# Kernel optimization log

Measured on AMD Instinct MI355X. Metric: run time of the kernel, lower is better.

## Reference

```python
import jax, jax.numpy as jnp
import numpy as np
from jax import lax


def setup_inputs() -> dict:
    key = jax.random.key(0)
    k1, k2 = jax.random.split(key)
    N, dim, m = 8192, 1024, 1024
    x = jax.random.normal(k1, (N, dim), dtype=jnp.float32)
    vectors = jax.random.normal(k2, (m, dim), dtype=jnp.float32) * 0.01
    bias = jnp.zeros((dim,), dtype=jnp.float32)
    return {"x": x, "vectors": vectors, "bias": bias}


def reference(x, vectors, bias):
    # Normalize each reflection vector to unit length: [m, d]
    v_normed = vectors / jnp.linalg.norm(vectors, axis=1, keepdims=True)

    def step(out, v):
        # out: [N, d], v: [d]
        proj = out @ v                       # [N]
        out = out - 2.0 * proj[:, None] * v  # rank-1 Householder update
        return out, None

    out, _ = lax.scan(step, x, v_normed)
    return out + bias
```

## Files before the change

kernel.cpp:

```cpp
#include <hip/hip_runtime.h>
#include <hip/hip_bf16.h>

typedef __attribute__((ext_vector_type(8))) short short8;
typedef __attribute__((ext_vector_type(4))) short s16x4;
typedef __attribute__((ext_vector_type(4))) float f32x4;

static __device__ inline short f2bf(float f) {
    unsigned u = __float_as_uint(f);
    unsigned r = (u + 0x7fffu + ((u >> 16) & 1u)) >> 16;
    return (short)r;
}
static __device__ inline float bf2f(short h) {
    return __uint_as_float(((unsigned)(unsigned short)h) << 16);
}

static __device__ inline int swz32(int row, int slot) {
    return row * 32 + ((slot ^ ((row >> 1) & 3)) << 3);
}
static __device__ inline int swz64(int row, int slot) {
    return row * 64 + ((slot ^ (row & 7)) << 3);
}

__global__ __launch_bounds__(256) void k_normalize(const float* __restrict__ vec,
                                                   float* __restrict__ V, int dim) {
    int row = blockIdx.x;
    const float4* src = (const float4*)(vec + (size_t)row * dim);
    float4* dst = (float4*)(V + (size_t)row * dim);
    int nv4 = dim >> 2;
    float ss = 0.f;
    for (int i = threadIdx.x; i < nv4; i += blockDim.x) {
        float4 v = src[i];
        ss += v.x * v.x + v.y * v.y + v.z * v.z + v.w * v.w;
    }
    for (int off = 32; off; off >>= 1) ss += __shfl_down(ss, off, 64);
    __shared__ float ws_[4];
    int lane = threadIdx.x & 63, w = threadIdx.x >> 6;
    if (lane == 0) ws_[w] = ss;
    __syncthreads();
    float inv = 1.0f / sqrtf(ws_[0] + ws_[1] + ws_[2] + ws_[3]);
    for (int i = threadIdx.x; i < nv4; i += blockDim.x) {
        float4 v = src[i];
        v.x *= inv; v.y *= inv; v.z *= inv; v.w *= inv;
        dst[i] = v;
    }
}

__global__ __launch_bounds__(256) void k_split(const float* __restrict__ X,
                                               short* __restrict__ Xh,
                                               short* __restrict__ Xl, int n4) {
    for (int i = blockIdx.x * blockDim.x + threadIdx.x; i < n4; i += gridDim.x * blockDim.x) {
        float4 v = ((const float4*)X)[i];
        float f[4] = {v.x, v.y, v.z, v.w};
        s16x4 h, l;
#pragma unroll
        for (int q = 0; q < 4; ++q) {
            h[q] = f2bf(f[q]);
            l[q] = f2bf(f[q] - bf2f(h[q]));
        }
        *(s16x4*)&Xh[(size_t)i * 4] = h;
        *(s16x4*)&Xl[(size_t)i * 4] = l;
    }
}

__global__ __launch_bounds__(256) void k_cast(const float* __restrict__ X,
                                              short* __restrict__ Xh, int n4) {
    for (int i = blockIdx.x * blockDim.x + threadIdx.x; i < n4; i += gridDim.x * blockDim.x) {
        float4 v = ((const float4*)X)[i];
        float f[4] = {v.x, v.y, v.z, v.w};
        s16x4 h;
#pragma unroll
        for (int q = 0; q < 4; ++q) h[q] = f2bf(f[q]);
        *(s16x4*)&Xh[(size_t)i * 4] = h;
    }
}

__global__ __launch_bounds__(256) void k_tsplit(const float* __restrict__ X,
                                                short* __restrict__ Xth,
                                                short* __restrict__ Xtl, int R, int C) {
    __shared__ float tile[32][33];
    int c0 = blockIdx.x * 32, r0 = blockIdx.y * 32;
    int t = threadIdx.x;
    int r = t >> 3, c4 = (t & 7) * 4;
    float4 v = *(const float4*)&X[(size_t)(r0 + r) * C + c0 + c4];
    tile[r][c4 + 0] = v.x; tile[r][c4 + 1] = v.y;
    tile[r][c4 + 2] = v.z; tile[r][c4 + 3] = v.w;
    __syncthreads();
    int rr = t >> 3, cc4 = (t & 7) * 4;
    s16x4 h, l;
#pragma unroll
    for (int q = 0; q < 4; ++q) {
        float f = tile[cc4 + q][rr];
        h[q] = f2bf(f);
        l[q] = f2bf(f - bf2f(h[q]));
    }
    *(s16x4*)&Xth[(size_t)(c0 + rr) * R + r0 + cc4] = h;
    *(s16x4*)&Xtl[(size_t)(c0 + rr) * R + r0 + cc4] = l;
}

template<int MODE, int TRI>
__global__ __launch_bounds__(256) void k_nt64(
    const short* __restrict__ Ah, const short* __restrict__ Al,
    const short* __restrict__ Bh, const short* __restrict__ Bl,
    float* __restrict__ Cf, short* __restrict__ Ch, short* __restrict__ Cl,
    int K, int lda, int ldb, int ldc) {
    __shared__ short As[2][64 * 32];
    __shared__ short Bs[2][64 * 32];
    int i0 = blockIdx.y * 64, j0 = blockIdx.x * 64;
    if (TRI == 2 && j0 < i0) return;
    int KE = (TRI == 1) ? (j0 + 64) : K;
    int t = threadIdx.x, lane = t & 63, wave = t >> 6;
    int wr = wave >> 1, wc = wave & 1;
    int srow = t >> 2, slot = t & 3;
    int sofs = swz32(srow, slot);
    int gofs = slot * 8;
    f32x4 acc[2][2] = {};
    for (int k0 = 0; k0 < KE; k0 += 32) {
        __syncthreads();
        *(short8*)&As[0][sofs] = *(const short8*)&Ah[(size_t)(i0 + srow) * lda + k0 + gofs];
        *(short8*)&As[1][sofs] = *(const short8*)&Al[(size_t)(i0 + srow) * lda + k0 + gofs];
        *(short8*)&Bs[0][sofs] = *(const short8*)&Bh[(size_t)(j0 + srow) * ldb + k0 + gofs];
        *(short8*)&Bs[1][sofs] = *(const short8*)&Bl[(size_t)(j0 + srow) * ldb + k0 + gofs];
        __syncthreads();
        int g = lane >> 4;
        short8 ah[2], al2[2], bh[2], bl2[2];
#pragma unroll
        for (int i = 0; i < 2; ++i) {
            int ro = swz32(wr * 32 + i * 16 + (lane & 15), g);
            ah[i] = *(const short8*)&As[0][ro];
            al2[i] = *(const short8*)&As[1][ro];
        }
#pragma unroll
        for (int j = 0; j < 2; ++j) {
            int ro = swz32(wc * 32 + j * 16 + (lane & 15), g);
            bh[j] = *(const short8*)&Bs[0][ro];
            bl2[j] = *(const short8*)&Bs[1][ro];
        }
#pragma unroll
        for (int i = 0; i < 2; ++i)
#pragma unroll
            for (int j = 0; j < 2; ++j) {
                acc[i][j] = __builtin_amdgcn_mfma_f32_16x16x32_bf16(ah[i], bh[j], acc[i][j], 0, 0, 0);
                acc[i][j] = __builtin_amdgcn_mfma_f32_16x16x32_bf16(ah[i], bl2[j], acc[i][j], 0, 0, 0);
                acc[i][j] = __builtin_amdgcn_mfma_f32_16x16x32_bf16(al2[i], bh[j], acc[i][j], 0, 0, 0);
            }
    }
#pragma unroll
    for (int i = 0; i < 2; ++i)
#pragma unroll
        for (int j = 0; j < 2; ++j) {
            int row0 = i0 + wr * 32 + i * 16 + ((lane >> 4) << 2);
            int col = j0 + wc * 32 + j * 16 + (lane & 15);
#pragma unroll
            for (int r = 0; r < 4; ++r) {
                float v = acc[i][j][r];
                size_t idx = (size_t)(row0 + r) * ldc + col;
                if (MODE == 2) {
                    Ch[idx] = f2bf((((row0 + r) == col) ? 1.f : 0.f) - v);
                } else {
                    short h = f2bf(v);
                    short l = f2bf(v - bf2f(h));
                    Ch[idx] = h;
                    Cl[idx] = l;
                    if (MODE == 3) Cf[idx] = v;
                }
            }
        }
}

__global__ __launch_bounds__(256) void k_baseinv2(const float* __restrict__ G,
                                                  short* __restrict__ Th, short* __restrict__ Tl,
                                                  short* __restrict__ Tth, short* __restrict__ Ttl,
                                                  int m) {
    __shared__ float Rs[64 * 64];
    int d = blockIdx.x >> 4, g = blockIdx.x & 15;
    int b0 = d * 64;
    int t = threadIdx.x, lane = t & 63, wave = t >> 6;
    {
        int r = t >> 2, c00 = (t & 3) * 16;
#pragma unroll
        for (int q = 0; q < 4; ++q)
            *(float4*)&Rs[r * 64 + c00 + q * 4] =
                *(const float4*)&G[(size_t)(b0 + r) * m + b0 + c00 + q * 4];
    }
    __syncthreads();
    int c = g * 4 + wave;
    float x = 0.f;
    for (int r = c; r >= 0; --r) {
        float prod = Rs[r * 64 + lane] * x;
        float s = prod;
#pragma unroll
        for (int off = 32; off; off >>= 1) s += __shfl_xor(s, off, 64);
        if (lane == r) x = ((r == c) ? 2.f : 0.f) - 2.f * s;
    }
    short h = f2bf(x);
    short l = f2bf(x - bf2f(h));
    Th[(size_t)(b0 + lane) * m + b0 + c] = h;
    Tl[(size_t)(b0 + lane) * m + b0 + c] = l;
    Tth[(size_t)(b0 + c) * m + b0 + lane] = h;
    Ttl[(size_t)(b0 + c) * m + b0 + lane] = l;
}

template<int PHASE>
__global__ __launch_bounds__(256) void k_trimm(
    const short* __restrict__ Ah, const short* __restrict__ Al,
    const short* __restrict__ Bh, const short* __restrict__ Bl,
    short* __restrict__ C1h, short* __restrict__ C1l,
    short* __restrict__ C2h, short* __restrict__ C2l,
    int m, int s) {
    __shared__ short As[2][64 * 32];
    __shared__ short Bs[2][64 * 32];
    int p = blockIdx.z;
    int a0 = 2 * p * s, c0 = a0 + s;
    int r0 = blockIdx.y * 64, ct = blockIdx.x * 64;
    int KS = (PHASE == 1) ? 0 : r0;
    int KE = (PHASE == 1) ? (ct + 64) : s;
    size_t tbase = (size_t)p * s * s;
    int t = threadIdx.x, lane = t & 63, wave = t >> 6;
    int wr = wave >> 1, wc = wave & 1;
    int srow = t >> 2, slot = t & 3;
    int sofs = swz32(srow, slot);
    int gofs = slot * 8;
    f32x4 acc[2][2] = {};
    for (int k0 = KS; k0 < KE; k0 += 32) {
        __syncthreads();
        if (PHASE == 1) {
            *(short8*)&As[0][sofs] = *(const short8*)&Ah[(size_t)(a0 + r0 + srow) * m + c0 + k0 + gofs];
            *(short8*)&As[1][sofs] = *(const short8*)&Al[(size_t)(a0 + r0 + srow) * m + c0 + k0 + gofs];
            *(short8*)&Bs[0][sofs] = *(const short8*)&Bh[(size_t)(c0 + ct + srow) * m + c0 + k0 + gofs];
            *(short8*)&Bs[1][sofs] = *(const short8*)&Bl[(size_t)(c0 + ct + srow) * m + c0 + k0 + gofs];
        } else {
            *(short8*)&As[0][sofs] = *(const short8*)&Ah[(size_t)(a0 + r0 + srow) * m + a0 + k0 + gofs];
            *(short8*)&As[1][sofs] = *(const short8*)&Al[(size_t)(a0 + r0 + srow) * m + a0 + k0 + gofs];
            *(short8*)&Bs[0][sofs] = *(const short8*)&Bh[tbase + (size_t)(ct + srow) * s + k0 + gofs];
            *(short8*)&Bs[1][sofs] = *(const short8*)&Bl[tbase + (size_t)(ct + srow) * s + k0 + gofs];
        }
        __syncthreads();
        int g = lane >> 4;
        short8 ah[2], al2[2], bh[2], bl2[2];
#pragma unroll
        for (int i = 0; i < 2; ++i) {
            int ro = swz32(wr * 32 + i * 16 + (lane & 15), g);
            ah[i] = *(const short8*)&As[0][ro];
            al2[i] = *(const short8*)&As[1][ro];
        }
#pragma unroll
        for (int j = 0; j < 2; ++j) {
            int ro = swz32(wc * 32 + j * 16 + (lane & 15), g);
            bh[j] = *(const short8*)&Bs[0][ro];
            bl2[j] = *(const short8*)&Bs[1][ro];
        }
#pragma unroll
        for (int i = 0; i < 2; ++i)
#pragma unroll
            for (int j = 0; j < 2; ++j) {
                acc[i][j] = __builtin_amdgcn_mfma_f32_16x16x32_bf16(ah[i], bh[j], acc[i][j], 0, 0, 0);
                acc[i][j] = __builtin_amdgcn_mfma_f32_16x16x32_bf16(ah[i], bl2[j], acc[i][j], 0, 0, 0);
                acc[i][j] = __builtin_amdgcn_mfma_f32_16x16x32_bf16(al2[i], bh[j], acc[i][j], 0, 0, 0);
            }
    }
#pragma unroll
    for (int i = 0; i < 2; ++i)
#pragma unroll
        for (int j = 0; j < 2; ++j) {
            int row0 = r0 + wr * 32 + i * 16 + ((lane >> 4) << 2);
            int col = ct + wc * 32 + j * 16 + (lane & 15);
#pragma unroll
            for (int r = 0; r < 4; ++r) {
                if (PHASE == 1) {
                    float v = acc[i][j][r];
                    short h = f2bf(v);
                    short l = f2bf(v - bf2f(h));
                    size_t idx = tbase + (size_t)col * s + row0 + r;
                    C1h[idx] = h;
                    C1l[idx] = l;
                } else {
                    float v = -acc[i][j][r];
                    short h = f2bf(v);
                    short l = f2bf(v - bf2f(h));
                    int R = a0 + row0 + r, Cc = c0 + col;
                    C1h[(size_t)R * m + Cc] = h;
                    C1l[(size_t)R * m + Cc] = l;
                    C2h[(size_t)Cc * m + R] = h;
                    C2l[(size_t)Cc * m + R] = l;
                }
            }
        }
}

__global__ __launch_bounds__(256) void k_apply3(const short* __restrict__ xh,
                                                const short* __restrict__ Qt,
                                                const float* __restrict__ bias,
                                                float* __restrict__ out, int dim) {
    __shared__ short As[128 * 64];
    __shared__ short Bs[128 * 64];
    int m0 = blockIdx.y * 128, n0 = blockIdx.x * 128;
    int t = threadIdx.x, lane = t & 63, wave = t >> 6;
    int wr = wave >> 1, wc = wave & 1;
    int sr = lane >> 3;
    int sslot = (lane & 7) ^ (sr & 7);
    f32x4 acc[4][4] = {};
    for (int k0 = 0; k0 < dim; k0 += 64) {
        __syncthreads();
#pragma unroll
        for (int q = 0; q < 4; ++q) {
            int rg = wave * 4 + q;
            int row = rg * 8 + sr;
            const short* gA = &xh[(size_t)(m0 + row) * dim + k0 + sslot * 8];
            const short* gB = &Qt[(size_t)(n0 + row) * dim + k0 + sslot * 8];
            __builtin_amdgcn_global_load_lds(
                (const __attribute__((address_space(1))) void*)gA,
                (__attribute__((address_space(3))) void*)&As[rg * 8 * 64], 16, 0, 0);
            __builtin_amdgcn_global_load_lds(
                (const __attribute__((address_space(1))) void*)gB,
                (__attribute__((address_space(3))) void*)&Bs[rg * 8 * 64], 16, 0, 0);
        }
        __syncthreads();
#pragma unroll
        for (int kk = 0; kk < 2; ++kk) {
            int g = kk * 4 + (lane >> 4);
            short8 af[4], bf_[4];
#pragma unroll
            for (int i = 0; i < 4; ++i)
                af[i] = *(const short8*)&As[swz64(wr * 64 + i * 16 + (lane & 15), g)];
#pragma unroll
            for (int j = 0; j < 4; ++j)
                bf_[j] = *(const short8*)&Bs[swz64(wc * 64 + j * 16 + (lane & 15), g)];
#pragma unroll
            for (int i = 0; i < 4; ++i)
#pragma unroll
                for (int j = 0; j < 4; ++j)
                    acc[i][j] = __builtin_amdgcn_mfma_f32_16x16x32_bf16(af[i], bf_[j], acc[i][j], 0, 0, 0);
        }
    }
#pragma unroll
    for (int i = 0; i < 4; ++i)
#pragma unroll
        for (int j = 0; j < 4; ++j) {
            int row = m0 + wr * 64 + i * 16 + (lane >> 4) * 4;
            int col = n0 + wc * 64 + j * 16 + (lane & 15);
            float b = bias[col];
#pragma unroll
            for (int r = 0; r < 4; ++r)
                out[(size_t)(row + r) * dim + col] = acc[i][j][r] + b;
        }
}

extern "C" void kernel_launch(void* const* d_in, const int* in_sizes, int n_in,
                              void* d_out, int out_size, void* d_ws, size_t ws_size,
                              hipStream_t stream) {
    const float* x = (const float*)d_in[0];
    const float* vec = (const float*)d_in[1];
    const float* bias = (const float*)d_in[2];
    float* out = (float*)d_out;

    int dim = in_sizes[2];
    int m = in_sizes[1] / dim;
    int n = in_sizes[0] / dim;

    const size_t MD = (size_t)m * dim;
    const size_t MM = (size_t)m * m;

    char* cur = (char*)d_ws;
    auto alloc_f = [&](size_t nelem) { float* p = (float*)cur; cur += nelem * 4; return p; };
    auto alloc_s = [&](size_t nelem) { short* p = (short*)cur; cur += nelem * 2; return p; };
    float* V   = alloc_f(MD);
    float* G   = alloc_f(MM);
    short* Vh  = alloc_s(MD);
    short* Vl  = alloc_s(MD);
    short* Vth = alloc_s(MD);
    short* Vtl = alloc_s(MD);
    short* Gh  = alloc_s(MM);
    short* Gl  = alloc_s(MM);
    short* Th  = alloc_s(MM);
    short* Tl  = alloc_s(MM);
    short* Tth = alloc_s(MM);
    short* Ttl = alloc_s(MM);
    short* Wh  = alloc_s(MD);
    short* Wl  = alloc_s(MD);
    short* Qt  = alloc_s((size_t)dim * dim);
    short* tmph = alloc_s(MM / 2);
    short* tmpl = alloc_s(MM / 2);
    short* xh  = alloc_s((size_t)n * dim);

    k_normalize<<<m, 256, 0, stream>>>(vec, V, dim);
    k_split<<<1024, 256, 0, stream>>>(V, Vh, Vl, (int)(MD / 4));
    k_tsplit<<<dim3(dim / 32, m / 32), 256, 0, stream>>>(V, Vth, Vtl, m, dim);

    k_nt64<3, 2><<<dim3(m / 64, m / 64), 256, 0, stream>>>(Vh, Vl, Vh, Vl, G, Gh, Gl,
                                                           dim, dim, dim, m);
    k_baseinv2<<<(m / 64) * 16, 256, 0, stream>>>(G, Th, Tl, Tth, Ttl, m);
    for (int s = 64; s < m; s <<= 1) {
        dim3 g(s / 64, s / 64, m / (2 * s));
        k_trimm<1><<<g, 256, 0, stream>>>(Gh, Gl, Tth, Ttl, tmph, tmpl, nullptr, nullptr, m, s);
        k_trimm<2><<<g, 256, 0, stream>>>(Th, Tl, tmph, tmpl, Th, Tl, Tth, Ttl, m, s);
    }

    k_nt64<1, 1><<<dim3(m / 64, dim / 64), 256, 0, stream>>>(Vth, Vtl, Tth, Ttl, nullptr, Wh, Wl,
                                                             m, m, m, m);
    k_nt64<2, 0><<<dim3(dim / 64, dim / 64), 256, 0, stream>>>(Vth, Vtl, Wh, Wl, nullptr, Qt, nullptr,
                                                               m, m, m, dim);

    k_cast<<<2048, 256, 0, stream>>>(x, xh, (int)((size_t)n * dim / 4));
    k_apply3<<<dim3(dim / 128, n / 128), 256, 0, stream>>>(xh, Qt, bias, out, dim);
}
```

Measured before the change: 178.9 us.

## Enlarge split-bf16 GEMM tiles to 128x128 with direct-to-LDS loads and XCD-swizzled apply grid

The small NT GEMMs that build the Gram matrix, W and Q now use 128x128 output tiles with a 4x4 MFMA grid per wave, and stage their tiles with global_load_lds instead of register round-trips. The apply kernel remaps its block index so consecutive tiles spread across the eight XCDs for better L2 locality. Larger tiles raise operand reuse and cut load instructions, but they give fewer blocks (64 or fewer) on a 256-CU part, which lowers occupancy and parallelism for these 1024-sized GEMMs.

```diff
diff --git a/kernel.cpp b/kernel.cpp
--- a/kernel.cpp
+++ b/kernel.cpp
@@ -98,58 +98,74 @@
 }
 
 template<int MODE, int TRI>
-__global__ __launch_bounds__(256) void k_nt64(
+__global__ __launch_bounds__(256) void k_nt128(
     const short* __restrict__ Ah, const short* __restrict__ Al,
     const short* __restrict__ Bh, const short* __restrict__ Bl,
     float* __restrict__ Cf, short* __restrict__ Ch, short* __restrict__ Cl,
     int K, int lda, int ldb, int ldc) {
-    __shared__ short As[2][64 * 32];
-    __shared__ short Bs[2][64 * 32];
-    int i0 = blockIdx.y * 64, j0 = blockIdx.x * 64;
+    __shared__ short Ash[128 * 32];
+    __shared__ short Asl[128 * 32];
+    __shared__ short Bsh[128 * 32];
+    __shared__ short Bsl[128 * 32];
+    int i0 = blockIdx.y * 128, j0 = blockIdx.x * 128;
     if (TRI == 2 && j0 < i0) return;
-    int KE = (TRI == 1) ? (j0 + 64) : K;
+    int KE = (TRI == 1) ? (j0 + 128) : K;
     int t = threadIdx.x, lane = t & 63, wave = t >> 6;
     int wr = wave >> 1, wc = wave & 1;
-    int srow = t >> 2, slot = t & 3;
-    int sofs = swz32(srow, slot);
-    int gofs = slot * 8;
-    f32x4 acc[2][2] = {};
+    int srIn = lane >> 2;
+    int sslot = (lane & 3) ^ ((lane >> 3) & 3);
+    f32x4 acc[4][4] = {};
     for (int k0 = 0; k0 < KE; k0 += 32) {
         __syncthreads();
-        *(short8*)&As[0][sofs] = *(const short8*)&Ah[(size_t)(i0 + srow) * lda + k0 + gofs];
-        *(short8*)&As[1][sofs] = *(const short8*)&Al[(size_t)(i0 + srow) * lda + k0 + gofs];
-        *(short8*)&Bs[0][sofs] = *(const short8*)&Bh[(size_t)(j0 + srow) * ldb + k0 + gofs];
-        *(short8*)&Bs[1][sofs] = *(const short8*)&Bl[(size_t)(j0 + srow) * ldb + k0 + gofs];
+#pragma unroll
+        for (int q = 0; q < 2; ++q) {
+            int rg = wave * 2 + q;
+            int row = rg * 16 + srIn;
+            size_t ga = (size_t)(i0 + row) * lda + k0 + sslot * 8;
+            size_t gb = (size_t)(j0 + row) * ldb + k0 + sslot * 8;
+            __builtin_amdgcn_global_load_lds(
+                (const __attribute__((address_space(1))) void*)&Ah[ga],
+                (__attribute__((address_space(3))) void*)&Ash[rg * 16 * 32], 16, 0, 0);
+            __builtin_amdgcn_global_load_lds(
+                (const __attribute__((address_space(1))) void*)&Al[ga],
+                (__attribute__((address_space(3))) void*)&Asl[rg * 16 * 32], 16, 0, 0);
+            __builtin_amdgcn_global_load_lds(
+                (const __attribute__((address_space(1))) void*)&Bh[gb],
+                (__attribute__((address_space(3))) void*)&Bsh[rg * 16 * 32], 16, 0, 0);
+            __builtin_amdgcn_global_load_lds(
+                (const __attribute__((address_space(1))) void*)&Bl[gb],
+                (__attribute__((address_space(3))) void*)&Bsl[rg * 16 * 32], 16, 0, 0);
+        }
         __syncthreads();
         int g = lane >> 4;
-        short8 ah[2], al2[2], bh[2], bl2[2];
-#pragma unroll
-        for (int i = 0; i < 2; ++i) {
-            int ro = swz32(wr * 32 + i * 16 + (lane & 15), g);
-            ah[i] = *(const short8*)&As[0][ro];
-            al2[i] = *(const short8*)&As[1][ro];
-        }
-#pragma unroll
-        for (int j = 0; j < 2; ++j) {
-            int ro = swz32(wc * 32 + j * 16 + (lane & 15), g);
-            bh[j] = *(const short8*)&Bs[0][ro];
-            bl2[j] = *(const short8*)&Bs[1][ro];
-        }
-#pragma unroll
-        for (int i = 0; i < 2; ++i)
-#pragma unroll
-            for (int j = 0; j < 2; ++j) {
+        short8 ah[4], al2[4], bh[4], bl2[4];
+#pragma unroll
+        for (int i = 0; i < 4; ++i) {
+            int ro = swz32(wr * 64 + i * 16 + (lane & 15), g);
+            ah[i] = *(const short8*)&Ash[ro];
+            al2[i] = *(const short8*)&Asl[ro];
+        }
+#pragma unroll
+        for (int j = 0; j < 4; ++j) {
+            int ro = swz32(wc * 64 + j * 16 + (lane & 15), g);
+            bh[j] = *(const short8*)&Bsh[ro];
+            bl2[j] = *(const short8*)&Bsl[ro];
+        }
+#pragma unroll
+        for (int i = 0; i < 4; ++i)
+#pragma unroll
+            for (int j = 0; j < 4; ++j) {
                 acc[i][j] = __builtin_amdgcn_mfma_f32_16x16x32_bf16(ah[i], bh[j], acc[i][j], 0, 0, 0);
                 acc[i][j] = __builtin_amdgcn_mfma_f32_16x16x32_bf16(ah[i], bl2[j], acc[i][j], 0, 0, 0);
                 acc[i][j] = __builtin_amdgcn_mfma_f32_16x16x32_bf16(al2[i], bh[j], acc[i][j], 0, 0, 0);
             }
     }
 #pragma unroll
-    for (int i = 0; i < 2; ++i)
-#pragma unroll
-        for (int j = 0; j < 2; ++j) {
-            int row0 = i0 + wr * 32 + i * 16 + ((lane >> 4) << 2);
-            int col = j0 + wc * 32 + j * 16 + (lane & 15);
+    for (int i = 0; i < 4; ++i)
+#pragma unroll
+        for (int j = 0; j < 4; ++j) {
+            int row0 = i0 + wr * 64 + i * 16 + ((lane >> 4) << 2);
+            int col = j0 + wc * 64 + j * 16 + (lane & 15);
 #pragma unroll
             for (int r = 0; r < 4; ++r) {
                 float v = acc[i][j][r];
@@ -293,7 +309,11 @@
                                                 float* __restrict__ out, int dim) {
     __shared__ short As[128 * 64];
     __shared__ short Bs[128 * 64];
-    int m0 = blockIdx.y * 128, n0 = blockIdx.x * 128;
+    int nwg = gridDim.x * gridDim.y;
+    int flat = blockIdx.y * gridDim.x + blockIdx.x;
+    int cpx = nwg >> 3;
+    int L = (flat & 7) * cpx + (flat >> 3);
+    int m0 = (L / gridDim.x) * 128, n0 = (L % gridDim.x) * 128;
     int t = threadIdx.x, lane = t & 63, wave = t >> 6;
     int wr = wave >> 1, wc = wave & 1;
     int sr = lane >> 3;
@@ -386,8 +406,8 @@
     k_split<<<1024, 256, 0, stream>>>(V, Vh, Vl, (int)(MD / 4));
     k_tsplit<<<dim3(dim / 32, m / 32), 256, 0, stream>>>(V, Vth, Vtl, m, dim);
 
-    k_nt64<3, 2><<<dim3(m / 64, m / 64), 256, 0, stream>>>(Vh, Vl, Vh, Vl, G, Gh, Gl,
-                                                           dim, dim, dim, m);
+    k_nt128<3, 2><<<dim3(m / 128, m / 128), 256, 0, stream>>>(Vh, Vl, Vh, Vl, G, Gh, Gl,
+                                                              dim, dim, dim, m);
     k_baseinv2<<<(m / 64) * 16, 256, 0, stream>>>(G, Th, Tl, Tth, Ttl, m);
     for (int s = 64; s < m; s <<= 1) {
         dim3 g(s / 64, s / 64, m / (2 * s));
@@ -395,10 +415,10 @@
         k_trimm<2><<<g, 256, 0, stream>>>(Th, Tl, tmph, tmpl, Th, Tl, Tth, Ttl, m, s);
     }
 
-    k_nt64<1, 1><<<dim3(m / 64, dim / 64), 256, 0, stream>>>(Vth, Vtl, Tth, Ttl, nullptr, Wh, Wl,
-                                                             m, m, m, m);
-    k_nt64<2, 0><<<dim3(dim / 64, dim / 64), 256, 0, stream>>>(Vth, Vtl, Wh, Wl, nullptr, Qt, nullptr,
-                                                               m, m, m, dim);
+    k_nt128<1, 1><<<dim3(m / 128, dim / 128), 256, 0, stream>>>(Vth, Vtl, Tth, Ttl, nullptr, Wh, Wl,
+                                                                m, m, m, m);
+    k_nt128<2, 0><<<dim3(dim / 128, dim / 128), 256, 0, stream>>>(Vth, Vtl, Wh, Wl, nullptr, Qt, nullptr,
+                                                                  m, m, m, dim);
 
     k_cast<<<2048, 256, 0, stream>>>(x, xh, (int)((size_t)n * dim / 4));
     k_apply3<<<dim3(dim / 128, n / 128), 256, 0, stream>>>(xh, Qt, bias, out, dim);
```

Result: slower. 235.7 us (+31.8%).
